# Performance work log

Measured on AMD Instinct MI355X. Metric: run time of the kernel, lower is better.

Reference implementation:

```python
import jax, jax.numpy as jnp
import numpy as np

B, T, HID = 2, 1024, 1024
NQ, NK, DK, DV = 8, 4, 128, 128
KDIM, KKDIM, KVDIM, VDIM = NQ * DK, NK * DK, NK * DV, NQ * DV  # 1024, 512, 512, 1024
CONV_DIM = KDIM + KKDIM + KVDIM  # 2048
KSZ = 4
EPS = 1e-5


def setup_inputs() -> dict:
    ks = jax.random.split(jax.random.key(0), 6)
    tot = KDIM + KKDIM + KVDIM + VDIM + NQ + NQ  # 3104
    return {
        "x": jax.random.normal(ks[0], (B, T, HID), jnp.float32),
        "w_in": jax.random.normal(ks[1], (HID, tot), jnp.float32) * 0.02,
        "conv_w": jax.random.normal(ks[2], (CONV_DIM, KSZ), jnp.float32) * 0.3,
        "A_log": jax.random.uniform(ks[3], (NQ,), jnp.float32, 0.0, 1.0),
        "dt_bias": jnp.ones((NQ,), jnp.float32),
        "norm_w": jnp.ones((DV,), jnp.float32),
        "w_out": jax.random.normal(ks[4], (VDIM, HID), jnp.float32) * 0.02,
    }


def _l2norm(u):
    return u * jax.lax.rsqrt(jnp.sum(u * u, axis=-1, keepdims=True) + 1e-6)


def _forward(x, w_in, conv_w, A_log, dt_bias, norm_w, w_out):
    # merged input projection -> q | k | v | z(gate) | b(beta) | a(decay)
    mixed = x @ w_in  # [B,T,3104]
    o1, o2, o3, o4, o5 = KDIM, KDIM + KKDIM, KDIM + KKDIM + KVDIM, KDIM + KKDIM + KVDIM + VDIM, KDIM + KKDIM + KVDIM + VDIM + NQ
    q, k, v, z, b, a = jnp.split(mixed, [o1, o2, o3, o4, o5], axis=-1)

    # short causal depthwise conv over concatenated q,k,v + silu
    qkv = jnp.concatenate([q, k, v], axis=-1)  # [B,T,CONV_DIM]
    pad = jnp.pad(qkv, ((0, 0), (KSZ - 1, 0), (0, 0)))
    conv = sum(pad[:, j:j + T, :] * conv_w[:, j] for j in range(KSZ))
    qkv = jax.nn.silu(conv)
    q, k, v = jnp.split(qkv, [KDIM, KDIM + KKDIM], axis=-1)

    q = q.reshape(B, T, NQ, DK)
    k = k.reshape(B, T, NK, DK)
    v = v.reshape(B, T, NK, DV)
    # GQA: repeat kv heads to q heads (kv_proj_rank is None -> plain repeat)
    rep = NQ // NK
    k = jnp.repeat(k, rep, axis=2)
    v = jnp.repeat(v, rep, axis=2)

    # qk l2-norm in kernel + query scaling
    q = _l2norm(q) * (DK ** -0.5)
    k = _l2norm(k)

    beta = jax.nn.sigmoid(b)                                # [B,T,NQ]
    g = -jnp.exp(A_log) * jax.nn.softplus(a + dt_bias)      # [B,T,NQ] log-decay

    tm = lambda u: jnp.moveaxis(u, 1, 0)  # time-major for scan

    def step(S, inp):
        # S: [B,NQ,DK,DV]
        qt, kt, vt, gt, bt = inp
        S = S * jnp.exp(gt)[..., None, None]
        vt = bt[..., None] * (vt - jnp.einsum('bhk,bhkv->bhv', kt, S))
        S = S + kt[..., None] * vt[..., None, :]
        ot = jnp.einsum('bhk,bhkv->bhv', qt, S)
        return S, ot

    S0 = jnp.zeros((B, NQ, DK, DV), x.dtype)
    _, o = jax.lax.scan(step, S0, (tm(q), tm(k), tm(v), tm(g), tm(beta)))
    o = jnp.moveaxis(o, 0, 1)  # [B,T,NQ,DV]

    # gated RMS norm with z, then output projection
    zz = z.reshape(B, T, NQ, DV)
    o = o * jax.lax.rsqrt(jnp.mean(o * o, axis=-1, keepdims=True) + EPS)
    o = o * norm_w * jax.nn.silu(zz)
    return o.reshape(B, T, VDIM) @ w_out


def reference(x, w_in, conv_w, A_log, dt_bias, norm_w, w_out):
    return _forward(x, w_in, conv_w, A_log, dt_bias, norm_w, w_out)
```

## Files before the change

### kernel.cpp

```cpp
#include <hip/hip_runtime.h>
#include <hip/hip_bf16.h>
#include <math.h>

#define BB    2
#define TT    1024
#define HID   1024
#define NQ    8
#define NK    4
#define DK    128
#define DV    128
#define TOT   3088
#define CONVD 2048
#define KSZ   4
#define BT    (BB*TT)
#define CHUNK 64
#define NCHUNK (TT/CHUNK)
#define NBH   (BB*NQ)
#define NPAD1 3200
#define JW    32

typedef __attribute__((ext_vector_type(8))) short short8v;
typedef __attribute__((ext_vector_type(4))) float f32x4;
typedef unsigned short ushort_t;
typedef unsigned int uint_t;

__device__ __forceinline__ float siluf(float x)     { return x / (1.f + expf(-x)); }
__device__ __forceinline__ float sigmoidf_(float x) { return 1.f / (1.f + expf(-x)); }
__device__ __forceinline__ float softplusf_(float x){ return x > 15.f ? x : log1pf(expf(x)); }

__device__ __forceinline__ ushort_t f2bf(float f) {
    uint_t u = __builtin_bit_cast(uint_t, f);
    u = (u + 0x7fff + ((u >> 16) & 1)) >> 16;
    return (ushort_t)u;
}
__device__ __forceinline__ float bf2f(ushort_t u) {
    uint_t v = ((uint_t)u) << 16;
    return __builtin_bit_cast(float, v);
}
__device__ __forceinline__ ushort4 pack4(f32x4 v) {
    ushort4 p; p.x = f2bf(v[0]); p.y = f2bf(v[1]); p.z = f2bf(v[2]); p.w = f2bf(v[3]);
    return p;
}

__device__ __forceinline__ void lds_barrier() {
    asm volatile("s_waitcnt lgkmcnt(0)" ::: "memory");
    __builtin_amdgcn_s_barrier();
}

__global__ __launch_bounds__(256) void f2bf_kernel(const float* __restrict__ src,
                                                   ushort_t* __restrict__ dst) {
    int i = (blockIdx.x * 256 + threadIdx.x) * 4;
    float4 v = *(const float4*)(src + i);
    ushort4 o;
    o.x = f2bf(v.x); o.y = f2bf(v.y); o.z = f2bf(v.z); o.w = f2bf(v.w);
    *(ushort4*)(dst + i) = o;
}

__global__ __launch_bounds__(256) void transpose_f2bf(const float* __restrict__ src,
                                                      ushort_t* __restrict__ dst,
                                                      int K, int N) {
    __shared__ float tile[32][33];
    int n0 = blockIdx.x * 32, k0 = blockIdx.y * 32;
    int c = threadIdx.x & 31, rbase = threadIdx.x >> 5;
    #pragma unroll
    for (int i = 0; i < 4; i++) {
        int r = rbase + i * 8;
        int n = n0 + c;
        tile[r][c] = (n < N) ? src[(size_t)(k0 + r) * N + n] : 0.f;
    }
    __syncthreads();
    #pragma unroll
    for (int i = 0; i < 4; i++) {
        int r = rbase + i * 8;
        dst[(size_t)(n0 + r) * K + k0 + c] = f2bf(tile[c][r]);
    }
}

__global__ __launch_bounds__(256) void gemm_bf16(const ushort_t* __restrict__ A,
                                                 const ushort_t* __restrict__ BTm,
                                                 float* __restrict__ C,
                                                 int K, int Nc, int ldc) {
    __shared__ ushort_t As[128 * 32];
    __shared__ ushort_t Bs[128 * 32];
    int tid = threadIdx.x;
    int wave = tid >> 6, lane = tid & 63;
    int wr = wave >> 1, wc = wave & 1;
    int row0 = blockIdx.y * 128, col0 = blockIdx.x * 128;

    f32x4 zero4 = {0.f, 0.f, 0.f, 0.f};
    f32x4 acc[4][4];
    #pragma unroll
    for (int m = 0; m < 4; m++)
        #pragma unroll
        for (int n = 0; n < 4; n++) acc[m][n] = zero4;

    int srow = wave * 32 + (lane >> 2);
    int koff = (lane & 3) * 8;
    const ushort_t* gA0 = A + (size_t)(row0 + srow) * K + koff;
    const ushort_t* gA1 = A + (size_t)(row0 + srow + 16) * K + koff;
    const ushort_t* gB0 = BTm + (size_t)(col0 + srow) * K + koff;
    const ushort_t* gB1 = BTm + (size_t)(col0 + srow + 16) * K + koff;
    ushort_t* lA0 = As + (wave * 2 + 0) * 512;
    ushort_t* lA1 = As + (wave * 2 + 1) * 512;
    ushort_t* lB0 = Bs + (wave * 2 + 0) * 512;
    ushort_t* lB1 = Bs + (wave * 2 + 1) * 512;

    for (int k0 = 0; k0 < K; k0 += 32) {
        __builtin_amdgcn_global_load_lds(
            (const __attribute__((address_space(1))) void*)(gA0 + k0),
            (__attribute__((address_space(3))) void*)lA0, 16, 0, 0);
        __builtin_amdgcn_global_load_lds(
            (const __attribute__((address_space(1))) void*)(gA1 + k0),
            (__attribute__((address_space(3))) void*)lA1, 16, 0, 0);
        __builtin_amdgcn_global_load_lds(
            (const __attribute__((address_space(1))) void*)(gB0 + k0),
            (__attribute__((address_space(3))) void*)lB0, 16, 0, 0);
        __builtin_amdgcn_global_load_lds(
            (const __attribute__((address_space(1))) void*)(gB1 + k0),
            (__attribute__((address_space(3))) void*)lB1, 16, 0, 0);
        __syncthreads();

        short8v af[4], bf[4];
        #pragma unroll
        for (int m = 0; m < 4; m++)
            af[m] = *(const short8v*)(As + (wr * 64 + m * 16 + (lane & 15)) * 32 + (lane >> 4) * 8);
        #pragma unroll
        for (int n = 0; n < 4; n++)
            bf[n] = *(const short8v*)(Bs + (wc * 64 + n * 16 + (lane & 15)) * 32 + (lane >> 4) * 8);
        #pragma unroll
        for (int m = 0; m < 4; m++)
            #pragma unroll
            for (int n = 0; n < 4; n++)
                acc[m][n] = __builtin_amdgcn_mfma_f32_16x16x32_bf16(af[m], bf[n], acc[m][n], 0, 0, 0);
        __syncthreads();
    }

    #pragma unroll
    for (int m = 0; m < 4; m++) {
        #pragma unroll
        for (int n = 0; n < 4; n++) {
            int row = row0 + wr * 64 + m * 16 + (lane >> 4) * 4;
            int col = col0 + wc * 64 + n * 16 + (lane & 15);
            if (col < Nc) {
                #pragma unroll
                for (int e = 0; e < 4; e++)
                    C[(size_t)(row + e) * ldc + col] = acc[m][n][e];
            }
        }
    }
}

__global__ __launch_bounds__(256) void conv_split_kernel(const float* __restrict__ mixed,
                                                         const float* __restrict__ conv_w,
                                                         const float* __restrict__ A_log,
                                                         const float* __restrict__ dt_bias,
                                                         ushort_t* __restrict__ qb,
                                                         ushort_t* __restrict__ kb,
                                                         float* __restrict__ kn,
                                                         float* __restrict__ vn,
                                                         float* __restrict__ beta,
                                                         float* __restrict__ g) {
    int bt = blockIdx.x;
    int t = bt & (TT - 1);
    int tid = threadIdx.x;
    int c0 = tid * 8;

    float val[8];
    #pragma unroll
    for (int i = 0; i < 8; i++) val[i] = 0.f;
    #pragma unroll
    for (int j = 0; j < KSZ; j++) {
        int tt = t - (KSZ - 1) + j;
        if (tt >= 0) {
            const float* src = mixed + (size_t)(bt - (KSZ - 1) + j) * TOT + c0;
            #pragma unroll
            for (int i = 0; i < 8; i++) val[i] += src[i] * conv_w[(c0 + i) * KSZ + j];
        }
    }
    #pragma unroll
    for (int i = 0; i < 8; i++) val[i] = siluf(val[i]);

    float ss = 0.f;
    #pragma unroll
    for (int i = 0; i < 8; i++) ss += val[i] * val[i];
    #pragma unroll
    for (int m = 1; m < 16; m <<= 1) ss += __shfl_xor(ss, m, 64);
    float rs = rsqrtf(ss + 1e-6f);

    if (tid < 128) {
        float sc = rs * 0.08838834764831845f;
        short8v pk;
        #pragma unroll
        for (int i = 0; i < 8; i++) pk[i] = (short)f2bf(val[i] * sc);
        *(short8v*)(qb + (size_t)bt * 1024 + c0) = pk;
    } else if (tid < 192) {
        int o = c0 - 1024;
        short8v pk;
        #pragma unroll
        for (int i = 0; i < 8; i++) {
            float kv = val[i] * rs;
            kn[(size_t)bt * 512 + o + i] = kv;
            pk[i] = (short)f2bf(kv);
        }
        *(short8v*)(kb + (size_t)bt * 512 + o) = pk;
    } else {
        #pragma unroll
        for (int i = 0; i < 8; i++) vn[(size_t)bt * 512 + (c0 - 1536) + i] = val[i];
    }
    if (tid < 8) {
        beta[bt * 8 + tid] = sigmoidf_(mixed[(size_t)bt * TOT + 3072 + tid]);
    } else if (tid < 16) {
        int h = tid - 8;
        g[bt * 8 + h] = -expf(A_log[h]) * softplusf_(mixed[(size_t)bt * TOT + 3080 + h] + dt_bias[h]);
    }
}

__global__ __launch_bounds__(256) void phaseA_kernel(const float* __restrict__ kn,
                                                     const float* __restrict__ vn,
                                                     const float* __restrict__ beta,
                                                     const float* __restrict__ g,
                                                     float* __restrict__ W,
                                                     ushort_t* __restrict__ Znegb,
                                                     ushort_t* __restrict__ knT,
                                                     float* __restrict__ Bvec) {
    int chunk = blockIdx.x;
    int bh = chunk >> 4, c = chunk & 15;
    int b = bh >> 3, h = bh & 7, hk = h >> 1;
    int bt0 = b * TT + c * CHUNK;
    int tid = threadIdx.x;
    int wave = tid >> 6, lane = tid & 63;
    int lr = lane & 15, lg = lane >> 4;

    __shared__ __align__(16) ushort_t kcb[64 * 128];
    __shared__ float Ms[64][65];
    __shared__ float Bv[64], Bev[64], bev[64];

    if (tid < 64) {
        float v = g[(size_t)(bt0 + tid) * 8 + h];
        #pragma unroll
        for (int off = 1; off < 64; off <<= 1) {
            float n = __shfl_up(v, off, 64);
            if (tid >= off) v += n;
        }
        Bv[tid] = v;
        Bev[tid] = expf(v);
        bev[tid] = beta[(size_t)(bt0 + tid) * 8 + h];
        Bvec[chunk * 64 + tid] = v;
    }
    for (int i = tid; i < 1024; i += 256) {
        int r = i >> 4, k16 = i & 15;
        const float* src = kn + (size_t)(bt0 + r) * 512 + hk * 128 + k16 * 8;
        float4 v0 = *(const float4*)src;
        float4 v1 = *(const float4*)(src + 4);
        short8v pk;
        pk[0] = (short)f2bf(v0.x); pk[1] = (short)f2bf(v0.y);
        pk[2] = (short)f2bf(v0.z); pk[3] = (short)f2bf(v0.w);
        pk[4] = (short)f2bf(v1.x); pk[5] = (short)f2bf(v1.y);
        pk[6] = (short)f2bf(v1.z); pk[7] = (short)f2bf(v1.w);
        int a = (r * 256 + k16 * 16) ^ ((r & 7) << 4);
        *(short8v*)((char*)kcb + a) = pk;
    }
    __syncthreads();

    {
        int t_lane = wave * 16 + lr;
        short8v af[4];
        #pragma unroll
        for (int ks = 0; ks < 4; ks++) {
            int a = (t_lane * 256 + ks * 64 + lg * 16) ^ ((t_lane & 7) << 4);
            af[ks] = *(const short8v*)((const char*)kcb + a);
        }
        for (int sb = 0; sb <= wave; sb++) {
            f32x4 macc = {0.f, 0.f, 0.f, 0.f};
            int s_lane = sb * 16 + lr;
            #pragma unroll
            for (int ks = 0; ks < 4; ks++) {
                int a = (s_lane * 256 + ks * 64 + lg * 16) ^ ((s_lane & 7) << 4);
                short8v bfr = *(const short8v*)((const char*)kcb + a);
                macc = __builtin_amdgcn_mfma_f32_16x16x32_bf16(af[ks], bfr, macc, 0, 0, 0);
            }
            #pragma unroll
            for (int e = 0; e < 4; e++) {
                int trow = wave * 16 + lg * 4 + e;
                int scol = sb * 16 + lr;
                Ms[trow][scol] = (scol < trow) ? macc[e] * bev[trow] * expf(Bv[trow] - Bv[scol]) : 0.f;
            }
        }
    }

    float Xr[64];
    if (tid < 128) {
        #pragma unroll
        for (int t = 0; t < 64; t++)
            Xr[t] = bev[t] * vn[(size_t)(bt0 + t) * 512 + hk * 128 + tid];
    } else {
        int r = tid - 128;
        #pragma unroll
        for (int t = 0; t < 64; t++)
            Xr[t] = bev[t] * Bev[t] * kn[(size_t)(bt0 + t) * 512 + hk * 128 + r];
    }
    __syncthreads();

    #pragma unroll
    for (int t = 1; t < 64; t++) {
        float a0 = 0.f, a1 = 0.f, a2 = 0.f, a3 = 0.f;
        #pragma unroll
        for (int s = 0; s + 4 <= t; s += 4) {
            a0 += Ms[t][s] * Xr[s];     a1 += Ms[t][s + 1] * Xr[s + 1];
            a2 += Ms[t][s + 2] * Xr[s + 2]; a3 += Ms[t][s + 3] * Xr[s + 3];
        }
        #pragma unroll
        for (int s = t & ~3; s < t; s++) a0 += Ms[t][s] * Xr[s];
        Xr[t] -= (a0 + a1) + (a2 + a3);
    }

    if (tid < 128) {
        float* Wc = W + (size_t)chunk * 8192 + tid;
        #pragma unroll
        for (int t = 0; t < 64; t++) Wc[t * 128] = Xr[t];
    } else {
        ushort_t* Zc = Znegb + (size_t)chunk * 8192 + (tid - 128);
        #pragma unroll
        for (int t = 0; t < 64; t++) Zc[t * 128] = f2bf(-Xr[t]);
    }

    if ((h & 1) == 0) {
        ushort_t* kT = knT + (size_t)(b * 4 + hk) * 131072 + c * 64;
        for (int i = tid; i < 8192; i += 256) {
            int r = i >> 6, tt = i & 63;
            int a = (tt * 256 + r * 2) ^ ((tt & 7) << 4);
            kT[(size_t)r * 1024 + tt] = *(const ushort_t*)((const char*)kcb + a);
        }
    }
}

__device__ __forceinline__ int swzSt(int j, int k) {
    int a = j * 256 + k * 2;
    return a ^ ((j & 7) << 4);
}
__device__ __forceinline__ int swzUt(int j, int s) {
    int a = j * 128 + s * 2;
    return a ^ ((j & 7) << 4);
}

__global__ __launch_bounds__(256) void phaseB_mfma(const ushort_t* __restrict__ knT,
                                                   const ushort_t* __restrict__ Znegb,
                                                   const float* __restrict__ W,
                                                   const float* __restrict__ Bvec,
                                                   ushort_t* __restrict__ SallT,
                                                   ushort_t* __restrict__ UTg) {
    int bh = blockIdx.x >> 2, cg = blockIdx.x & 3;
    int b = bh >> 3, h = bh & 7, hk = h >> 1;
    int j0 = cg * JW;
    int tid = threadIdx.x;
    int wave = tid >> 6, lane = tid & 63;
    int lr = lane & 15, lg = lane >> 4;
    int t0 = wave * 16;

    __shared__ __align__(16) ushort_t St[JW * 128];
    __shared__ __align__(16) ushort_t Ut[JW * 64];

    for (int i = tid * 8; i < JW * 128; i += 2048)
        *(int4*)(St + i) = make_int4(0, 0, 0, 0);

    f32x4 Sacc[2][2];
    #pragma unroll
    for (int fr = 0; fr < 2; fr++)
        #pragma unroll
        for (int fc = 0; fc < 2; fc++) Sacc[fr][fc] = (f32x4){0.f, 0.f, 0.f, 0.f};

    const ushort_t* kTbase = knT + (size_t)(b * 4 + hk) * 131072;
    int chunk0 = bh * 16;

    short8v za[4], ka[4];
    f32x4 wv[2];
    f32x4 bvv[4];
    float b63;
    {
        const ushort_t* Zc = Znegb + (size_t)chunk0 * 8192;
        #pragma unroll
        for (int ks = 0; ks < 4; ks++)
            za[ks] = *(const short8v*)(Zc + (size_t)(t0 + lr) * 128 + ks * 32 + lg * 8);
        const float* Wc = W + (size_t)chunk0 * 8192 + j0;
        #pragma unroll
        for (int fc = 0; fc < 2; fc++)
            #pragma unroll
            for (int e = 0; e < 4; e++)
                wv[fc][e] = Wc[(size_t)(t0 + lg * 4 + e) * 128 + fc * 16 + lr];
        #pragma unroll
        for (int fr = 0; fr < 2; fr++)
            #pragma unroll
            for (int ss = 0; ss < 2; ss++)
                ka[fr * 2 + ss] = *(const short8v*)(kTbase +
                    (size_t)(wave * 32 + fr * 16 + lr) * 1024 + ss * 32 + lg * 8);
        #pragma unroll
        for (int q = 0; q < 4; q++)
            bvv[q] = *(const f32x4*)(Bvec + chunk0 * 64 + (q >> 1) * 32 + lg * 8 + (q & 1) * 4);
        b63 = Bvec[chunk0 * 64 + 63];
    }

    for (int c = 0; c < NCHUNK; c++) {
        int chunk = chunk0 + c;
        ushort_t* SgT = SallT + (size_t)chunk * 16384;
        #pragma unroll
        for (int fr = 0; fr < 2; fr++)
            #pragma unroll
            for (int fc = 0; fc < 2; fc++) {
                int r0 = wave * 32 + fr * 16 + lg * 4;
                int j = j0 + fc * 16 + lr;
                *(ushort4*)(SgT + (size_t)j * 128 + r0) = pack4(Sacc[fr][fc]);
            }
        f32x4 Uacc[2];
        Uacc[0] = wv[0];
        Uacc[1] = wv[1];

        lds_barrier();

        #pragma unroll
        for (int ks = 0; ks < 4; ks++)
            #pragma unroll
            for (int fc = 0; fc < 2; fc++) {
                short8v sb = *(const short8v*)((const char*)St + swzSt(fc * 16 + lr, ks * 32 + lg * 8));
                Uacc[fc] = __builtin_amdgcn_mfma_f32_16x16x32_bf16(za[ks], sb, Uacc[fc], 0, 0, 0);
            }
        ushort_t* UTc = UTg + (size_t)chunk * 8192;
        #pragma unroll
        for (int fc = 0; fc < 2; fc++) {
            int jl = fc * 16 + lr;
            ushort4 pu = pack4(Uacc[fc]);
            *(ushort4*)(UTc + (size_t)(j0 + jl) * 64 + t0 + lg * 4) = pu;
            *(ushort4*)((char*)Ut + swzUt(jl, t0 + lg * 4)) = pu;
        }
        if (c + 1 < NCHUNK) {
            const ushort_t* Zn = Znegb + (size_t)(chunk + 1) * 8192;
            #pragma unroll
            for (int ks = 0; ks < 4; ks++)
                za[ks] = *(const short8v*)(Zn + (size_t)(t0 + lr) * 128 + ks * 32 + lg * 8);
            const float* Wn = W + (size_t)(chunk + 1) * 8192 + j0;
            #pragma unroll
            for (int fc = 0; fc < 2; fc++)
                #pragma unroll
                for (int e = 0; e < 4; e++)
                    wv[fc][e] = Wn[(size_t)(t0 + lg * 4 + e) * 128 + fc * 16 + lr];
        }
        float gC = expf(b63);
        #pragma unroll
        for (int fr = 0; fr < 2; fr++)
            #pragma unroll
            for (int fc = 0; fc < 2; fc++)
                #pragma unroll
                for (int e = 0; e < 4; e++) Sacc[fr][fc][e] *= gC;

        lds_barrier();

        float eb[2][8];
        #pragma unroll
        for (int ss = 0; ss < 2; ss++)
            #pragma unroll
            for (int e = 0; e < 8; e++)
                eb[ss][e] = expf(b63 - bvv[ss * 2 + (e >> 2)][e & 3]);

        #pragma unroll
        for (int fr = 0; fr < 2; fr++) {
            #pragma unroll
            for (int ss = 0; ss < 2; ss++) {
                short8v a;
                #pragma unroll
                for (int e = 0; e < 8; e++)
                    a[e] = (short)f2bf(bf2f((ushort_t)ka[fr * 2 + ss][e]) * eb[ss][e]);
                #pragma unroll
                for (int fc = 0; fc < 2; fc++) {
                    short8v ub = *(const short8v*)((const char*)Ut + swzUt(fc * 16 + lr, ss * 32 + lg * 8));
                    Sacc[fr][fc] = __builtin_amdgcn_mfma_f32_16x16x32_bf16(a, ub, Sacc[fr][fc], 0, 0, 0);
                }
            }
        }
        if (c + 1 < NCHUNK) {
            #pragma unroll
            for (int fr = 0; fr < 2; fr++)
                #pragma unroll
                for (int ss = 0; ss < 2; ss++)
                    ka[fr * 2 + ss] = *(const short8v*)(kTbase +
                        (size_t)(wave * 32 + fr * 16 + lr) * 1024 + (c + 1) * 64 + ss * 32 + lg * 8);
            #pragma unroll
            for (int q = 0; q < 4; q++)
                bvv[q] = *(const f32x4*)(Bvec + (chunk + 1) * 64 + (q >> 1) * 32 + lg * 8 + (q & 1) * 4);
            b63 = Bvec[(chunk + 1) * 64 + 63];
        }
        #pragma unroll
        for (int fr = 0; fr < 2; fr++)
            #pragma unroll
            for (int fc = 0; fc < 2; fc++) {
                int r = wave * 32 + fr * 16 + lg * 4;
                int j = fc * 16 + lr;
                *(ushort4*)((char*)St + swzSt(j, r)) = pack4(Sacc[fr][fc]);
            }
    }
}

__global__ __launch_bounds__(256) void phaseC_mfma(const ushort_t* __restrict__ qb,
                                                   const ushort_t* __restrict__ kb,
                                                   const ushort_t* __restrict__ UTg,
                                                   const ushort_t* __restrict__ SallT,
                                                   const float* __restrict__ Bvec,
                                                   float* __restrict__ o) {
    int chunk = blockIdx.x;
    int bh = chunk >> 4, c = chunk & 15;
    int b = bh >> 3, h = bh & 7, hk = h >> 1;
    int bt0 = b * TT + c * CHUNK;
    int tid = threadIdx.x, wave = tid >> 6, lane = tid & 63;
    int lr = lane & 15, lg = lane >> 4;

    __shared__ float Bv[64], Bev[64];
    __shared__ __align__(16) ushort_t Pb[64 * 64];

    if (tid < 64) { float v = Bvec[chunk * 64 + tid]; Bv[tid] = v; Bev[tid] = expf(v); }
    __syncthreads();

    int t_lane = wave * 16 + lr;
    const ushort_t* qrow = qb + (size_t)(bt0 + t_lane) * 1024 + h * 128;
    short8v qa[4];
    #pragma unroll
    for (int ks = 0; ks < 4; ks++) qa[ks] = *(const short8v*)(qrow + ks * 32 + lg * 8);

    #pragma unroll
    for (int sb = 0; sb < 4; sb++) {
        f32x4 pacc = {0.f, 0.f, 0.f, 0.f};
        const ushort_t* krow = kb + (size_t)(bt0 + sb * 16 + lr) * 512 + hk * 128;
        #pragma unroll
        for (int ks = 0; ks < 4; ks++) {
            short8v kf = *(const short8v*)(krow + ks * 32 + lg * 8);
            pacc = __builtin_amdgcn_mfma_f32_16x16x32_bf16(qa[ks], kf, pacc, 0, 0, 0);
        }
        int scol = sb * 16 + lr;
        #pragma unroll
        for (int e = 0; e < 4; e++) {
            int trow = wave * 16 + lg * 4 + e;
            float val = (scol <= trow) ? pacc[e] * expf(Bv[trow] - Bv[scol]) : 0.f;
            int a = (trow * 128 + scol * 2) ^ ((trow & 7) << 4);
            *(ushort_t*)((char*)Pb + a) = f2bf(val);
        }
    }

    float Ge[4];
    #pragma unroll
    for (int e = 0; e < 4; e++) Ge[e] = Bev[wave * 16 + lg * 4 + e];
    const ushort_t* ST = SallT + (size_t)chunk * 16384;
    f32x4 acc[8];
    #pragma unroll
    for (int n = 0; n < 8; n++) {
        acc[n] = (f32x4){0.f, 0.f, 0.f, 0.f};
        int j = n * 16 + lr;
        #pragma unroll
        for (int rs = 0; rs < 4; rs++) {
            short8v sf = *(const short8v*)(ST + (size_t)j * 128 + rs * 32 + lg * 8);
            acc[n] = __builtin_amdgcn_mfma_f32_16x16x32_bf16(qa[rs], sf, acc[n], 0, 0, 0);
        }
        #pragma unroll
        for (int e = 0; e < 4; e++) acc[n][e] *= Ge[e];
    }
    __syncthreads();

    short8v pa[2];
    #pragma unroll
    for (int ks = 0; ks < 2; ks++) {
        int a = (t_lane * 128 + (ks * 32 + lg * 8) * 2) ^ ((t_lane & 7) << 4);
        pa[ks] = *(const short8v*)((const char*)Pb + a);
    }
    const ushort_t* UTc = UTg + (size_t)chunk * 8192;
    #pragma unroll
    for (int n = 0; n < 8; n++) {
        int j = n * 16 + lr;
        #pragma unroll
        for (int ks = 0; ks < 2; ks++) {
            short8v uf = *(const short8v*)(UTc + (size_t)j * 64 + ks * 32 + lg * 8);
            acc[n] = __builtin_amdgcn_mfma_f32_16x16x32_bf16(pa[ks], uf, acc[n], 0, 0, 0);
        }
    }
    #pragma unroll
    for (int n = 0; n < 8; n++) {
        int j = n * 16 + lr;
        #pragma unroll
        for (int e = 0; e < 4; e++) {
            int t = wave * 16 + lg * 4 + e;
            o[(size_t)(bt0 + t) * 1024 + h * 128 + j] = acc[n][e];
        }
    }
}

__global__ __launch_bounds__(64) void norm_gate_kernel(const float* __restrict__ o_scan,
                                                       const float* __restrict__ mixed,
                                                       const float* __restrict__ norm_w,
                                                       ushort_t* __restrict__ ginb) {
    int bth = blockIdx.x;
    int bt = bth >> 3, h = bth & 7;
    int lane = threadIdx.x;
    size_t base = (size_t)bt * 1024 + h * 128;
    float o0 = o_scan[base + lane];
    float o1 = o_scan[base + lane + 64];
    float ss = o0 * o0 + o1 * o1;
    #pragma unroll
    for (int m = 1; m < 64; m <<= 1) ss += __shfl_xor(ss, m, 64);
    float r = rsqrtf(ss * (1.f / 128.f) + 1e-5f);
    size_t zbase = (size_t)bt * TOT + 2048 + h * 128;
    float z0 = mixed[zbase + lane];
    float z1 = mixed[zbase + lane + 64];
    ginb[base + lane]      = f2bf(o0 * r * norm_w[lane]      * siluf(z0));
    ginb[base + lane + 64] = f2bf(o1 * r * norm_w[lane + 64] * siluf(z1));
}

extern "C" void kernel_launch(void* const* d_in, const int* in_sizes, int n_in,
                              void* d_out, int out_size, void* d_ws, size_t ws_size,
                              hipStream_t stream) {
    const float* x       = (const float*)d_in[0];
    const float* w_in    = (const float*)d_in[1];
    const float* conv_w  = (const float*)d_in[2];
    const float* A_log   = (const float*)d_in[3];
    const float* dt_bias = (const float*)d_in[4];
    const float* norm_w  = (const float*)d_in[5];
    const float* w_out   = (const float*)d_in[6];
    float* out = (float*)d_out;

    float* ws = (float*)d_ws;
    float* mixed = ws;
    float* kn    = mixed + (size_t)BT * TOT;
    float* vn    = kn + (size_t)BT * 512;
    float* beta  = vn + (size_t)BT * 512;
    float* gdec  = beta + BT * 8;
    float* Wu    = gdec + BT * 8;
    float* Bvec  = Wu + (size_t)BT * 1024;
    float* qbf   = Bvec + NBH * NCHUNK * 64;
    float* kbf   = qbf + 1048576;
    float* knTf  = kbf + 524288;
    float* Znf   = knTf + 524288;
    float* UTf   = Znf + 1048576;
    float* SallTf= UTf + 1048576;
    float* bt2f  = SallTf + 2097152;

    ushort_t* qb    = (ushort_t*)qbf;
    ushort_t* kb    = (ushort_t*)kbf;
    ushort_t* knTb  = (ushort_t*)knTf;
    ushort_t* Znegb = (ushort_t*)Znf;
    ushort_t* UTb   = (ushort_t*)UTf;
    ushort_t* SallT = (ushort_t*)SallTf;
    ushort_t* bt2   = (ushort_t*)bt2f;
    ushort_t* xb    = (ushort_t*)SallTf;
    ushort_t* bt1   = (ushort_t*)knTf;
    ushort_t* ginb  = (ushort_t*)qbf;
    float* oscan    = Wu;

    f2bf_kernel<<<(BT * HID) / 1024, 256, 0, stream>>>(x, xb);
    transpose_f2bf<<<dim3(NPAD1 / 32, HID / 32), 256, 0, stream>>>(w_in, bt1, HID, TOT);
    transpose_f2bf<<<dim3(HID / 32, HID / 32), 256, 0, stream>>>(w_out, bt2, HID, HID);

    gemm_bf16<<<dim3(NPAD1 / 128, BT / 128), 256, 0, stream>>>(xb, bt1, mixed, HID, TOT, TOT);

    conv_split_kernel<<<BT, 256, 0, stream>>>(mixed, conv_w, A_log, dt_bias, qb, kb, kn, vn, beta, gdec);

    phaseA_kernel<<<NBH * NCHUNK, 256, 0, stream>>>(kn, vn, beta, gdec, Wu, Znegb, knTb, Bvec);
    phaseB_mfma<<<NBH * 4, 256, 0, stream>>>(knTb, Znegb, Wu, Bvec, SallT, UTb);
    phaseC_mfma<<<NBH * NCHUNK, 256, 0, stream>>>(qb, kb, UTb, SallT, Bvec, oscan);

    norm_gate_kernel<<<BT * NQ, 64, 0, stream>>>(oscan, mixed, norm_w, ginb);

    gemm_bf16<<<dim3(HID / 128, BT / 128), 256, 0, stream>>>(ginb, bt2, out, HID, HID, HID);
}
```

Baseline: 186.2 us.

## Merge prep kernels, remap chunk block order, per-head knT, batch norm-gate blocks

The three preprocessing launches (x cast and the two weight transposes) become one prep_kernel, which saves launch overhead. phaseA, phaseB and phaseC now interleave heads across block indices (bh = blockIdx & 15) so concurrent blocks cover different heads. The k-transpose buffer knT is now written per q-head instead of only by even heads, which doubles that buffer and its writes but removes the predicate. norm_gate packs four rows per 256-thread block to cut block count.

```diff
diff --git a/kernel.cpp b/kernel.cpp
--- a/kernel.cpp
+++ b/kernel.cpp
@@ -47,20 +47,11 @@
     __builtin_amdgcn_s_barrier();
 }
 
-__global__ __launch_bounds__(256) void f2bf_kernel(const float* __restrict__ src,
-                                                   ushort_t* __restrict__ dst) {
-    int i = (blockIdx.x * 256 + threadIdx.x) * 4;
-    float4 v = *(const float4*)(src + i);
-    ushort4 o;
-    o.x = f2bf(v.x); o.y = f2bf(v.y); o.z = f2bf(v.z); o.w = f2bf(v.w);
-    *(ushort4*)(dst + i) = o;
-}
-
-__global__ __launch_bounds__(256) void transpose_f2bf(const float* __restrict__ src,
-                                                      ushort_t* __restrict__ dst,
-                                                      int K, int N) {
+__device__ __forceinline__ void transpose_body(const float* __restrict__ src,
+                                               ushort_t* __restrict__ dst,
+                                               int K, int N, int bx, int by) {
     __shared__ float tile[32][33];
-    int n0 = blockIdx.x * 32, k0 = blockIdx.y * 32;
+    int n0 = bx * 32, k0 = by * 32;
     int c = threadIdx.x & 31, rbase = threadIdx.x >> 5;
     #pragma unroll
     for (int i = 0; i < 4; i++) {
@@ -73,6 +64,28 @@
     for (int i = 0; i < 4; i++) {
         int r = rbase + i * 8;
         dst[(size_t)(n0 + r) * K + k0 + c] = f2bf(tile[c][r]);
+    }
+}
+
+__global__ __launch_bounds__(256) void prep_kernel(const float* __restrict__ x,
+                                                   const float* __restrict__ w_in,
+                                                   const float* __restrict__ w_out,
+                                                   ushort_t* __restrict__ xb,
+                                                   ushort_t* __restrict__ bt1,
+                                                   ushort_t* __restrict__ bt2) {
+    int bid = blockIdx.x;
+    if (bid < 2048) {
+        int i = (bid * 256 + threadIdx.x) * 4;
+        float4 v = *(const float4*)(x + i);
+        ushort4 o;
+        o.x = f2bf(v.x); o.y = f2bf(v.y); o.z = f2bf(v.z); o.w = f2bf(v.w);
+        *(ushort4*)(xb + i) = o;
+    } else if (bid < 2048 + 3200) {
+        int t = bid - 2048;
+        transpose_body(w_in, bt1, HID, TOT, t % 100, t / 100);
+    } else {
+        int t = bid - 5248;
+        transpose_body(w_out, bt2, HID, HID, t % 32, t / 32);
     }
 }
 
@@ -223,8 +236,8 @@
                                                      ushort_t* __restrict__ Znegb,
                                                      ushort_t* __restrict__ knT,
                                                      float* __restrict__ Bvec) {
-    int chunk = blockIdx.x;
-    int bh = chunk >> 4, c = chunk & 15;
+    int bh = blockIdx.x & 15, c = blockIdx.x >> 4;
+    int chunk = bh * 16 + c;
     int b = bh >> 3, h = bh & 7, hk = h >> 1;
     int bt0 = b * TT + c * CHUNK;
     int tid = threadIdx.x;
@@ -324,8 +337,8 @@
         for (int t = 0; t < 64; t++) Zc[t * 128] = f2bf(-Xr[t]);
     }
 
-    if ((h & 1) == 0) {
-        ushort_t* kT = knT + (size_t)(b * 4 + hk) * 131072 + c * 64;
+    {
+        ushort_t* kT = knT + (size_t)bh * 131072 + c * 64;
         for (int i = tid; i < 8192; i += 256) {
             int r = i >> 6, tt = i & 63;
             int a = (tt * 256 + r * 2) ^ ((tt & 7) << 4);
@@ -349,8 +362,7 @@
                                                    const float* __restrict__ Bvec,
                                                    ushort_t* __restrict__ SallT,
                                                    ushort_t* __restrict__ UTg) {
-    int bh = blockIdx.x >> 2, cg = blockIdx.x & 3;
-    int b = bh >> 3, h = bh & 7, hk = h >> 1;
+    int bh = blockIdx.x & 15, cg = blockIdx.x >> 4;
     int j0 = cg * JW;
     int tid = threadIdx.x;
     int wave = tid >> 6, lane = tid & 63;
@@ -369,7 +381,7 @@
         #pragma unroll
         for (int fc = 0; fc < 2; fc++) Sacc[fr][fc] = (f32x4){0.f, 0.f, 0.f, 0.f};
 
-    const ushort_t* kTbase = knT + (size_t)(b * 4 + hk) * 131072;
+    const ushort_t* kTbase = knT + (size_t)bh * 131072;
     int chunk0 = bh * 16;
 
     short8v za[4], ka[4];
@@ -504,8 +516,8 @@
                                                    const ushort_t* __restrict__ SallT,
                                                    const float* __restrict__ Bvec,
                                                    float* __restrict__ o) {
-    int chunk = blockIdx.x;
-    int bh = chunk >> 4, c = chunk & 15;
+    int bh = blockIdx.x & 15, c = blockIdx.x >> 4;
+    int chunk = bh * 16 + c;
     int b = bh >> 3, h = bh & 7, hk = h >> 1;
     int bt0 = b * TT + c * CHUNK;
     int tid = threadIdx.x, wave = tid >> 6, lane = tid & 63;
@@ -588,13 +600,13 @@
     }
 }
 
-__global__ __launch_bounds__(64) void norm_gate_kernel(const float* __restrict__ o_scan,
-                                                       const float* __restrict__ mixed,
-                                                       const float* __restrict__ norm_w,
-                                                       ushort_t* __restrict__ ginb) {
-    int bth = blockIdx.x;
+__global__ __launch_bounds__(256) void norm_gate_kernel(const float* __restrict__ o_scan,
+                                                        const float* __restrict__ mixed,
+                                                        const float* __restrict__ norm_w,
+                                                        ushort_t* __restrict__ ginb) {
+    int bth = blockIdx.x * 4 + (threadIdx.x >> 6);
     int bt = bth >> 3, h = bth & 7;
-    int lane = threadIdx.x;
+    int lane = threadIdx.x & 63;
     size_t base = (size_t)bt * 1024 + h * 128;
     float o0 = o_scan[base + lane];
     float o1 = o_scan[base + lane + 64];
@@ -632,7 +644,7 @@
     float* qbf   = Bvec + NBH * NCHUNK * 64;
     float* kbf   = qbf + 1048576;
     float* knTf  = kbf + 524288;
-    float* Znf   = knTf + 524288;
+    float* Znf   = knTf + 1048576;
     float* UTf   = Znf + 1048576;
     float* SallTf= UTf + 1048576;
     float* bt2f  = SallTf + 2097152;
@@ -649,9 +661,7 @@
     ushort_t* ginb  = (ushort_t*)qbf;
     float* oscan    = Wu;
 
-    f2bf_kernel<<<(BT * HID) / 1024, 256, 0, stream>>>(x, xb);
-    transpose_f2bf<<<dim3(NPAD1 / 32, HID / 32), 256, 0, stream>>>(w_in, bt1, HID, TOT);
-    transpose_f2bf<<<dim3(HID / 32, HID / 32), 256, 0, stream>>>(w_out, bt2, HID, HID);
+    prep_kernel<<<6272, 256, 0, stream>>>(x, w_in, w_out, xb, bt1, bt2);
 
     gemm_bf16<<<dim3(NPAD1 / 128, BT / 128), 256, 0, stream>>>(xb, bt1, mixed, HID, TOT, TOT);
 
@@ -661,7 +671,7 @@
     phaseB_mfma<<<NBH * 4, 256, 0, stream>>>(knTb, Znegb, Wu, Bvec, SallT, UTb);
     phaseC_mfma<<<NBH * NCHUNK, 256, 0, stream>>>(qb, kb, UTb, SallT, Bvec, oscan);
 
-    norm_gate_kernel<<<BT * NQ, 64, 0, stream>>>(oscan, mixed, norm_w, ginb);
+    norm_gate_kernel<<<BT * NQ / 4, 256, 0, stream>>>(oscan, mixed, norm_w, ginb);
 
     gemm_bf16<<<dim3(HID / 128, BT / 128), 256, 0, stream>>>(ginb, bt2, out, HID, HID, HID);
 }
```

Result: faster. 180.3 us (-3.2%).
